# Performance work log

Hardware: AMD Instinct MI355X
Metric: run time of the kernel (lower is better)

## Reference

```python
import jax, jax.numpy as jnp
import numpy as np

DT = 0.1  # fixed Euler base step, as in the torch module
B, D, H = 65536, 64, 128


def setup_inputs() -> dict:
    key = jax.random.key(0)
    ks = jax.random.split(key, 9)
    z = jax.random.normal(ks[0], (B, D), dtype=jnp.float32)
    # time_delta in [-2, 2) -> steps = ceil(max|td|/0.1) ~= 20
    time_delta = jax.random.uniform(ks[1], (B,), dtype=jnp.float32, minval=-2.0, maxval=2.0)

    def lin_init(kw, kb, fan_in, fan_out):
        bound = 1.0 / np.sqrt(fan_in)
        W = jax.random.uniform(kw, (fan_in, fan_out), jnp.float32, -bound, bound)
        b = jax.random.uniform(kb, (fan_out,), jnp.float32, -bound, bound)
        return W, b

    W1, b1 = lin_init(ks[2], ks[3], D + 1, H)
    W2, b2 = lin_init(ks[4], ks[5], H, H)
    W3, b3 = lin_init(ks[6], ks[7], H, D)
    return dict(z=z, time_delta=time_delta, W1=W1, b1=b1, W2=W2, b2=b2, W3=W3, b3=b3)


def reference(z, time_delta, W1, b1, W2, b2, W3, b3):
    # steps is derived from concrete input data (as in the torch .item() call)
    steps = int(np.ceil(float(jnp.max(jnp.abs(time_delta))) / DT))
    if steps == 0:
        return z
    actual_dt = (time_delta / steps)[:, None]          # [B, 1]
    ts = jnp.arange(steps, dtype=z.dtype) * DT         # time feature per step (scalar, batch-uniform)

    Wz, Wt = W1[:-1], W1[-1]  # concat([z, t*ones]) @ W1 == z @ Wz + t * Wt

    def step(z_c, t):
        h = jnp.tanh(z_c @ Wz + t * Wt + b1)           # [B, H]
        h = jnp.tanh(h @ W2 + b2)                      # [B, H]
        dz = h @ W3 + b3                               # [B, D]
        return z_c + dz * actual_dt, None

    z_final, _ = jax.lax.scan(step, z, ts)
    return z_final
```

## Files before the change

### kernel.cpp

```cpp
#include <hip/hip_runtime.h>

#define B_N 65536
#define D_N 64
#define H_N 128

typedef __attribute__((ext_vector_type(8))) __bf16 bf16x8;
typedef __attribute__((ext_vector_type(8))) unsigned short ushort8;
typedef __attribute__((ext_vector_type(4))) float f32x4;
typedef __attribute__((ext_vector_type(4))) unsigned int uint32x4;


__device__ __forceinline__ unsigned short f2bf(float f) {
    unsigned u = __float_as_uint(f);
    u += 0x7FFFu + ((u >> 16) & 1u);
    return (unsigned short)(u >> 16);
}

__device__ __forceinline__ float fast_tanh(float x) {
    float e = __expf(2.0f * x);
    return fmaf(-2.0f, __builtin_amdgcn_rcpf(e + 1.0f), 1.0f);
}

__device__ __forceinline__ unsigned cvt_pk_bf16(float lo, float hi) {
    unsigned r;
    asm("v_cvt_pk_bf16_f32 %0, %1, %2" : "=v"(r) : "v"(lo), "v"(hi));
    return r;
}

__device__ __forceinline__ int sigma(int m) {
    return (m & 96) | ((m & 4) << 2) | ((m >> 1) & 12) | (m & 3);
}

__device__ __forceinline__ bf16x8 ldsfrag(const unsigned short* p) {
    return __builtin_bit_cast(bf16x8, *(const ushort8*)p);
}

__global__ void k_pre(const float* __restrict__ td, const float* __restrict__ W1,
                      const float* __restrict__ W2, const float* __restrict__ W3,
                      unsigned* __restrict__ ws) {
    if (blockIdx.x < 64) {
        int i = blockIdx.x * blockDim.x + threadIdx.x;
        float m = 0.0f;
        for (; i < B_N; i += 64 * 256) m = fmaxf(m, fabsf(td[i]));
#pragma unroll
        for (int o = 32; o; o >>= 1) m = fmaxf(m, __shfl_down(m, o));
        if ((threadIdx.x & 63) == 0) atomicMax(ws, __float_as_uint(m));
    } else {
        int i = (blockIdx.x - 64) * 256 + threadIdx.x;
        unsigned short* wsb = (unsigned short*)(ws + 16);
        float v;
        if (i < 8192) {
            int n = i >> 6, m = i & 63;
            v = W1[sigma(m) * 128 + n];
        } else if (i < 24576) {
            int o = i - 8192;
            int n = o >> 7, m = o & 127;
            v = W2[sigma(m) * 128 + n];
        } else {
            int o = i - 24576;
            int n = o >> 7, m = o & 127;
            v = W3[sigma(m) * 64 + n];
        }
        wsb[i] = f2bf(v);
    }
}

__launch_bounds__(256, 2)
__global__ void k_main(const float* __restrict__ z_in, const float* __restrict__ td,
                       const float* __restrict__ W1, const float* __restrict__ b1,
                       const float* __restrict__ b2, const float* __restrict__ b3,
                       const void* __restrict__ ws, float* __restrict__ out) {
    __shared__ unsigned short WzL[128 * 96];
    __shared__ unsigned short W3L[64 * 136];

    const unsigned* wsu = (const unsigned*)ws;
    const unsigned short* wzg = (const unsigned short*)((const char*)ws + 64);
    const unsigned short* w2g = wzg + 8192;
    const unsigned short* w3g = wzg + 24576;

    const int tid = threadIdx.x;

    for (int c = tid; c < 1024; c += 256) {
        int r = c >> 3, k8 = (c & 7) << 3;
        *(ushort8*)&WzL[r * 96 + k8] = *(const ushort8*)&wzg[r * 64 + k8];
    }
    for (int n = tid; n < 128; n += 256) {
        WzL[n * 96 + 64] = f2bf(W1[64 * 128 + n]);
        WzL[n * 96 + 65] = f2bf(b1[n]);
        unsigned* pz = (unsigned*)&WzL[n * 96 + 66];
#pragma unroll
        for (int k = 0; k < 15; ++k) pz[k] = 0u;
    }
    for (int c = tid; c < 1024; c += 256) {
        int r = c >> 4, k8 = (c & 15) << 3;
        *(ushort8*)&W3L[r * 136 + k8] = *(const ushort8*)&w3g[r * 128 + k8];
    }
    __syncthreads();

    const float maxab = __uint_as_float(wsu[0]);
    const int steps = (int)ceil((double)maxab / 0.1);

    const int wave = tid >> 6;
    const int lane = tid & 63;
    const int q = lane >> 4;
    const int m15 = lane & 15;

    bf16x8 w2f[8][4];
#pragma unroll
    for (int n0 = 0; n0 < 8; ++n0)
#pragma unroll
        for (int kt = 0; kt < 4; ++kt)
            w2f[n0][kt] = __builtin_bit_cast(
                bf16x8, *(const ushort8*)&w2g[(n0 * 16 + m15) * 128 + kt * 32 + q * 8]);

    f32x4 b2c[8];
#pragma unroll
    for (int n0 = 0; n0 < 8; ++n0)
        b2c[n0] = *(const f32x4*)&b2[n0 * 16 + q * 4];

    const unsigned short* wzbase = &WzL[m15 * 96 + q * 8];
    const unsigned short* w3base = &W3L[m15 * 136 + q * 8];

    for (int tile = 0; tile < 2; ++tile) {
        const int row = (blockIdx.x * 2 + tile) * 64 + wave * 16 + m15;

        float zr[16];
#pragma unroll
        for (int kt = 0; kt < 2; ++kt)
#pragma unroll
            for (int hi = 0; hi < 2; ++hi) {
                f32x4 v = *(const f32x4*)(z_in + (size_t)row * 64 + kt * 32 + hi * 16 + q * 4);
#pragma unroll
                for (int r = 0; r < 4; ++r) zr[kt * 8 + hi * 4 + r] = v[r];
            }
        const float tdr = td[row];
        const float dtr = (steps > 0) ? (tdr / (float)steps) : 0.0f;

        for (int s = 0; s < steps; ++s) {
            const float t = (float)s * 0.1f;

            unsigned za[8];
#pragma unroll
            for (int i = 0; i < 8; ++i) za[i] = cvt_pk_bf16(zr[2 * i], zr[2 * i + 1]);
            unsigned tw = cvt_pk_bf16(t, 1.0f);
            tw = (q == 0) ? tw : 0u;
            bf16x8 zA0 = __builtin_bit_cast(bf16x8, (uint32x4){za[0], za[1], za[2], za[3]});
            bf16x8 zA1 = __builtin_bit_cast(bf16x8, (uint32x4){za[4], za[5], za[6], za[7]});
            bf16x8 zA2 = __builtin_bit_cast(bf16x8, (uint32x4){tw, 0u, 0u, 0u});

            unsigned hv[16];
#pragma unroll
            for (int n0 = 0; n0 < 8; ++n0) {
                f32x4 acc = {0.f, 0.f, 0.f, 0.f};
                acc = __builtin_amdgcn_mfma_f32_16x16x32_bf16(
                    ldsfrag(wzbase + n0 * 1536), zA0, acc, 0, 0, 0);
                acc = __builtin_amdgcn_mfma_f32_16x16x32_bf16(
                    ldsfrag(wzbase + n0 * 1536 + 32), zA1, acc, 0, 0, 0);
                acc = __builtin_amdgcn_mfma_f32_16x16x32_bf16(
                    ldsfrag(wzbase + n0 * 1536 + 64), zA2, acc, 0, 0, 0);
                hv[n0 * 2 + 0] = cvt_pk_bf16(fast_tanh(acc[0]), fast_tanh(acc[1]));
                hv[n0 * 2 + 1] = cvt_pk_bf16(fast_tanh(acc[2]), fast_tanh(acc[3]));
            }

            unsigned gv[16];
#pragma unroll
            for (int n0 = 0; n0 < 8; ++n0) {
                f32x4 acc = b2c[n0];
#pragma unroll
                for (int kt = 0; kt < 4; ++kt) {
                    bf16x8 hf = __builtin_bit_cast(
                        bf16x8, (uint32x4){hv[4 * kt], hv[4 * kt + 1],
                                           hv[4 * kt + 2], hv[4 * kt + 3]});
                    acc = __builtin_amdgcn_mfma_f32_16x16x32_bf16(w2f[n0][kt], hf, acc, 0, 0, 0);
                }
                gv[n0 * 2 + 0] = cvt_pk_bf16(fast_tanh(acc[0]), fast_tanh(acc[1]));
                gv[n0 * 2 + 1] = cvt_pk_bf16(fast_tanh(acc[2]), fast_tanh(acc[3]));
            }

#pragma unroll
            for (int n0 = 0; n0 < 4; ++n0) {
                f32x4 acc = {0.f, 0.f, 0.f, 0.f};
#pragma unroll
                for (int kt = 0; kt < 4; ++kt) {
                    bf16x8 gf = __builtin_bit_cast(
                        bf16x8, (uint32x4){gv[4 * kt], gv[4 * kt + 1],
                                           gv[4 * kt + 2], gv[4 * kt + 3]});
                    acc = __builtin_amdgcn_mfma_f32_16x16x32_bf16(
                        ldsfrag(w3base + n0 * 2176 + kt * 32), gf, acc, 0, 0, 0);
                }
#pragma unroll
                for (int r = 0; r < 4; ++r)
                    zr[n0 * 4 + r] = fmaf(acc[r], dtr, zr[n0 * 4 + r]);
            }
        }

#pragma unroll
        for (int n0 = 0; n0 < 4; ++n0) {
            f32x4 bb = *(const f32x4*)&b3[n0 * 16 + q * 4];
#pragma unroll
            for (int r = 0; r < 4; ++r)
                zr[n0 * 4 + r] = fmaf(tdr, bb[r], zr[n0 * 4 + r]);
        }

#pragma unroll
        for (int kt = 0; kt < 2; ++kt)
#pragma unroll
            for (int hi = 0; hi < 2; ++hi) {
                f32x4 v;
#pragma unroll
                for (int r = 0; r < 4; ++r) v[r] = zr[kt * 8 + hi * 4 + r];
                *(f32x4*)(out + (size_t)row * 64 + kt * 32 + hi * 16 + q * 4) = v;
            }
    }
}

extern "C" void kernel_launch(void* const* d_in, const int* in_sizes, int n_in,
                              void* d_out, int out_size, void* d_ws, size_t ws_size,
                              hipStream_t stream) {
    const float* z  = (const float*)d_in[0];
    const float* td = (const float*)d_in[1];
    const float* W1 = (const float*)d_in[2];
    const float* b1 = (const float*)d_in[3];
    const float* W2 = (const float*)d_in[4];
    const float* b2 = (const float*)d_in[5];
    const float* W3 = (const float*)d_in[6];
    const float* b3 = (const float*)d_in[7];
    float* out = (float*)d_out;
    (void)in_sizes; (void)n_in; (void)out_size; (void)ws_size;

    hipMemsetAsync(d_ws, 0, 64, stream);
    k_pre<<<192, 256, 0, stream>>>(td, W1, W2, W3, (unsigned*)d_ws);
    k_main<<<512, 256, 0, stream>>>(z, td, W1, b1, b2, b3, d_ws, out);
}
```

Measured before the change: 217.9 us.

## Keep all weight fragments in registers, fold tanh scale into weights, fewer blocks

Removes the LDS staging of Wz and W3. All weight fragments (Wz, W2, W3 and an augmented time/bias fragment) now sit in VGPRs, which cuts LDS reads inside the step loop. The 2/ln2 factor is folded into W1, W2, b1 and b2 so tanh can use raw v_exp_f32 without a multiply. In exchange, occupancy drops to one block per CU: launch bounds go to 1, the grid halves to 256 blocks, and each block handles 4 tiles. This risks less latency hiding and possible register spills, and on a 256-CU part it leaves only one wave per SIMD.

After: 208.5 us. -4.3%, faster.

```diff
diff --git a/kernel.cpp b/kernel.cpp
--- a/kernel.cpp
+++ b/kernel.cpp
@@ -3,6 +3,7 @@
 #define B_N 65536
 #define D_N 64
 #define H_N 128
+#define K_SCALE 2.885390081777927f
 
 typedef __attribute__((ext_vector_type(8))) __bf16 bf16x8;
 typedef __attribute__((ext_vector_type(8))) unsigned short ushort8;
@@ -16,8 +17,9 @@
     return (unsigned short)(u >> 16);
 }
 
-__device__ __forceinline__ float fast_tanh(float x) {
-    float e = __expf(2.0f * x);
+__device__ __forceinline__ float tanh_scaled(float a) {
+    float e;
+    asm("v_exp_f32 %0, %1" : "=v"(e) : "v"(a));
     return fmaf(-2.0f, __builtin_amdgcn_rcpf(e + 1.0f), 1.0f);
 }
 
@@ -29,10 +31,6 @@
 
 __device__ __forceinline__ int sigma(int m) {
     return (m & 96) | ((m & 4) << 2) | ((m >> 1) & 12) | (m & 3);
-}
-
-__device__ __forceinline__ bf16x8 ldsfrag(const unsigned short* p) {
-    return __builtin_bit_cast(bf16x8, *(const ushort8*)p);
 }
 
 __global__ void k_pre(const float* __restrict__ td, const float* __restrict__ W1,
@@ -51,11 +49,11 @@
         float v;
         if (i < 8192) {
             int n = i >> 6, m = i & 63;
-            v = W1[sigma(m) * 128 + n];
+            v = W1[sigma(m) * 128 + n] * K_SCALE;
         } else if (i < 24576) {
             int o = i - 8192;
             int n = o >> 7, m = o & 127;
-            v = W2[sigma(m) * 128 + n];
+            v = W2[sigma(m) * 128 + n] * K_SCALE;
         } else {
             int o = i - 24576;
             int n = o >> 7, m = o & 127;
@@ -65,64 +63,68 @@
     }
 }
 
-__launch_bounds__(256, 2)
+__launch_bounds__(256, 1)
 __global__ void k_main(const float* __restrict__ z_in, const float* __restrict__ td,
                        const float* __restrict__ W1, const float* __restrict__ b1,
                        const float* __restrict__ b2, const float* __restrict__ b3,
                        const void* __restrict__ ws, float* __restrict__ out) {
-    __shared__ unsigned short WzL[128 * 96];
-    __shared__ unsigned short W3L[64 * 136];
-
     const unsigned* wsu = (const unsigned*)ws;
     const unsigned short* wzg = (const unsigned short*)((const char*)ws + 64);
     const unsigned short* w2g = wzg + 8192;
     const unsigned short* w3g = wzg + 24576;
 
     const int tid = threadIdx.x;
-
-    for (int c = tid; c < 1024; c += 256) {
-        int r = c >> 3, k8 = (c & 7) << 3;
-        *(ushort8*)&WzL[r * 96 + k8] = *(const ushort8*)&wzg[r * 64 + k8];
-    }
-    for (int n = tid; n < 128; n += 256) {
-        WzL[n * 96 + 64] = f2bf(W1[64 * 128 + n]);
-        WzL[n * 96 + 65] = f2bf(b1[n]);
-        unsigned* pz = (unsigned*)&WzL[n * 96 + 66];
-#pragma unroll
-        for (int k = 0; k < 15; ++k) pz[k] = 0u;
-    }
-    for (int c = tid; c < 1024; c += 256) {
-        int r = c >> 4, k8 = (c & 15) << 3;
-        *(ushort8*)&W3L[r * 136 + k8] = *(const ushort8*)&w3g[r * 128 + k8];
-    }
-    __syncthreads();
-
-    const float maxab = __uint_as_float(wsu[0]);
-    const int steps = (int)ceil((double)maxab / 0.1);
-
     const int wave = tid >> 6;
     const int lane = tid & 63;
     const int q = lane >> 4;
     const int m15 = lane & 15;
 
+    bf16x8 wzf[8][2];
     bf16x8 w2f[8][4];
+    bf16x8 w3f[4][4];
+    bf16x8 augf[8];
+#pragma unroll
+    for (int n0 = 0; n0 < 8; ++n0)
+#pragma unroll
+        for (int kt = 0; kt < 2; ++kt)
+            wzf[n0][kt] = __builtin_bit_cast(
+                bf16x8, *(const ushort8*)&wzg[(n0 * 16 + m15) * 64 + kt * 32 + q * 8]);
 #pragma unroll
     for (int n0 = 0; n0 < 8; ++n0)
 #pragma unroll
         for (int kt = 0; kt < 4; ++kt)
             w2f[n0][kt] = __builtin_bit_cast(
                 bf16x8, *(const ushort8*)&w2g[(n0 * 16 + m15) * 128 + kt * 32 + q * 8]);
+#pragma unroll
+    for (int n0 = 0; n0 < 4; ++n0)
+#pragma unroll
+        for (int kt = 0; kt < 4; ++kt)
+            w3f[n0][kt] = __builtin_bit_cast(
+                bf16x8, *(const ushort8*)&w3g[(n0 * 16 + m15) * 128 + kt * 32 + q * 8]);
+#pragma unroll
+    for (int n0 = 0; n0 < 8; ++n0) {
+        const int n = n0 * 16 + m15;
+        float wt = W1[64 * 128 + n] * K_SCALE;
+        float bb = b1[n] * K_SCALE;
+        unsigned w = (unsigned)f2bf(wt) | ((unsigned)f2bf(bb) << 16);
+        w = (q == 0) ? w : 0u;
+        augf[n0] = __builtin_bit_cast(bf16x8, (uint32x4){w, 0u, 0u, 0u});
+    }
 
     f32x4 b2c[8];
 #pragma unroll
-    for (int n0 = 0; n0 < 8; ++n0)
-        b2c[n0] = *(const f32x4*)&b2[n0 * 16 + q * 4];
-
-    const unsigned short* wzbase = &WzL[m15 * 96 + q * 8];
-    const unsigned short* w3base = &W3L[m15 * 136 + q * 8];
-
-    for (int tile = 0; tile < 2; ++tile) {
-        const int row = (blockIdx.x * 2 + tile) * 64 + wave * 16 + m15;
+    for (int n0 = 0; n0 < 8; ++n0) {
+        f32x4 v = *(const f32x4*)&b2[n0 * 16 + q * 4];
+#pragma unroll
+        for (int r = 0; r < 4; ++r) v[r] *= K_SCALE;
+        b2c[n0] = v;
+    }
+
+    const float maxab = __uint_as_float(wsu[0]);
+    const int steps = (int)ceil((double)maxab / 0.1);
+
+    for (int tile = 0; tile < 4; ++tile) {
+        const int row = blockIdx.x * 256 + tile * 64 + wave * 16 + m15;
 
         float zr[16];
 #pragma unroll
@@ -152,14 +154,11 @@
 #pragma unroll
             for (int n0 = 0; n0 < 8; ++n0) {
                 f32x4 acc = {0.f, 0.f, 0.f, 0.f};
-                acc = __builtin_amdgcn_mfma_f32_16x16x32_bf16(
-                    ldsfrag(wzbase + n0 * 1536), zA0, acc, 0, 0, 0);
-                acc = __builtin_amdgcn_mfma_f32_16x16x32_bf16(
-                    ldsfrag(wzbase + n0 * 1536 + 32), zA1, acc, 0, 0, 0);
-                acc = __builtin_amdgcn_mfma_f32_16x16x32_bf16(
-                    ldsfrag(wzbase + n0 * 1536 + 64), zA2, acc, 0, 0, 0);
-                hv[n0 * 2 + 0] = cvt_pk_bf16(fast_tanh(acc[0]), fast_tanh(acc[1]));
-                hv[n0 * 2 + 1] = cvt_pk_bf16(fast_tanh(acc[2]), fast_tanh(acc[3]));
+                acc = __builtin_amdgcn_mfma_f32_16x16x32_bf16(wzf[n0][0], zA0, acc, 0, 0, 0);
+                acc = __builtin_amdgcn_mfma_f32_16x16x32_bf16(wzf[n0][1], zA1, acc, 0, 0, 0);
+                acc = __builtin_amdgcn_mfma_f32_16x16x32_bf16(augf[n0],   zA2, acc, 0, 0, 0);
+                hv[n0 * 2 + 0] = cvt_pk_bf16(tanh_scaled(acc[0]), tanh_scaled(acc[1]));
+                hv[n0 * 2 + 1] = cvt_pk_bf16(tanh_scaled(acc[2]), tanh_scaled(acc[3]));
             }
 
             unsigned gv[16];
@@ -173,8 +172,8 @@
                                            hv[4 * kt + 2], hv[4 * kt + 3]});
                     acc = __builtin_amdgcn_mfma_f32_16x16x32_bf16(w2f[n0][kt], hf, acc, 0, 0, 0);
                 }
-                gv[n0 * 2 + 0] = cvt_pk_bf16(fast_tanh(acc[0]), fast_tanh(acc[1]));
-                gv[n0 * 2 + 1] = cvt_pk_bf16(fast_tanh(acc[2]), fast_tanh(acc[3]));
+                gv[n0 * 2 + 0] = cvt_pk_bf16(tanh_scaled(acc[0]), tanh_scaled(acc[1]));
+                gv[n0 * 2 + 1] = cvt_pk_bf16(tanh_scaled(acc[2]), tanh_scaled(acc[3]));
             }
 
 #pragma unroll
@@ -185,8 +184,7 @@
                     bf16x8 gf = __builtin_bit_cast(
                         bf16x8, (uint32x4){gv[4 * kt], gv[4 * kt + 1],
                                            gv[4 * kt + 2], gv[4 * kt + 3]});
-                    acc = __builtin_amdgcn_mfma_f32_16x16x32_bf16(
-                        ldsfrag(w3base + n0 * 2176 + kt * 32), gf, acc, 0, 0, 0);
+                    acc = __builtin_amdgcn_mfma_f32_16x16x32_bf16(w3f[n0][kt], gf, acc, 0, 0, 0);
                 }
 #pragma unroll
                 for (int r = 0; r < 4; ++r)
@@ -194,12 +192,13 @@
             }
         }
 
+        const float tb3 = (steps > 0) ? tdr : 0.0f;
 #pragma unroll
         for (int n0 = 0; n0 < 4; ++n0) {
             f32x4 bb = *(const f32x4*)&b3[n0 * 16 + q * 4];
 #pragma unroll
             for (int r = 0; r < 4; ++r)
-                zr[n0 * 4 + r] = fmaf(tdr, bb[r], zr[n0 * 4 + r]);
+                zr[n0 * 4 + r] = fmaf(tb3, bb[r], zr[n0 * 4 + r]);
         }
 
 #pragma unroll
@@ -230,5 +229,5 @@
 
     hipMemsetAsync(d_ws, 0, 64, stream);
     k_pre<<<192, 256, 0, stream>>>(td, W1, W2, W3, (unsigned*)d_ws);
-    k_main<<<512, 256, 0, stream>>>(z, td, W1, b1, b2, b3, d_ws, out);
-}
+    k_main<<<256, 256, 0, stream>>>(z, td, W1, b1, b2, b3, d_ws, out);
+}
```
